# Performance work log

Measured on AMD Instinct MI355X. Metric: run time of the kernel, lower is better.

Reference implementation:

```python
import jax, jax.numpy as jnp
import numpy as np

INPUT_DIM = 1024
DAY_EMB = 8
PRED_LEN = 96
HIDDEN = 512
BATCH = 4096


def setup_inputs() -> dict:
    key = jax.random.key(0)
    ks = jax.random.split(key, 6)
    x = jax.random.normal(ks[0], (BATCH, INPUT_DIM), dtype=jnp.float32)
    day_emb = jax.random.normal(ks[1], (PRED_LEN, DAY_EMB), dtype=jnp.float32)
    # stacked per-head first-layer weights: in = input_dim + day_emb_dim
    W1 = jax.random.normal(ks[2], (PRED_LEN, INPUT_DIM + DAY_EMB, HIDDEN), dtype=jnp.float32) * 0.02
    b1 = jax.random.normal(ks[3], (PRED_LEN, HIDDEN), dtype=jnp.float32) * 0.02
    # stacked per-head output Linear(hidden, 1) weights (squeezed)
    W2 = jax.random.normal(ks[4], (PRED_LEN, HIDDEN), dtype=jnp.float32) * 0.02
    b2 = jax.random.normal(ks[5], (PRED_LEN,), dtype=jnp.float32) * 0.02
    return {"x": x, "day_emb": day_emb, "W1": W1, "b1": b1, "W2": W2, "b2": b2}


def reference(x, day_emb, W1, b1, W2, b2):
    # Each head p sees f = concat([x, day_emb[p]]) -> Linear -> ReLU -> (Dropout eval=id) -> Linear(.,1)
    # Split W1 into the x-part and emb-part so we never materialize the [P,B,in+emb] concat.
    W1x = W1[:, :INPUT_DIM, :]          # [P, D, H]
    W1e = W1[:, INPUT_DIM:, :]          # [P, E, H]
    h = jnp.einsum('bd,pdh->pbh', x, W1x)  # [P, B, H]
    h = h + (jnp.einsum('pe,peh->ph', day_emb, W1e) + b1)[:, None, :]
    h = jax.nn.relu(h)
    out = jnp.einsum('pbh,ph->pb', h, W2) + b2[:, None]  # [P, B]
    return out.T  # [B, pred_len]
```

## Files before the change

### kernel.cpp

```cpp
#include <hip/hip_runtime.h>
#include <hip/hip_bf16.h>
#include <stdint.h>

#define INPUT_DIM 1024
#define PRED_LEN 96
#define HIDDEN 512
#define BATCH 4096
#define W1_ROWS 1032

typedef __attribute__((ext_vector_type(8))) short bf16x8;
typedef __attribute__((ext_vector_type(4))) float floatx4;

__device__ __forceinline__ unsigned short f32_to_bf16_rne(float f) {
    union { float f; unsigned int u; } v; v.f = f;
    unsigned int u = v.u;
    unsigned int r = u + 0x7fffu + ((u >> 16) & 1u);
    return (unsigned short)(r >> 16);
}

__device__ __forceinline__ void async_copy16(const void* g, void* l) {
    __builtin_amdgcn_global_load_lds(
        (const __attribute__((address_space(1))) unsigned int*)g,
        (__attribute__((address_space(3))) unsigned int*)l, 16, 0, 0);
}

__global__ void convert_x_kernel(const float* __restrict__ x,
                                 unsigned short* __restrict__ xb) {
    int i = (blockIdx.x * 256 + threadIdx.x) * 4;
    float4 v = *reinterpret_cast<const float4*>(x + i);
    ushort4 o;
    o.x = f32_to_bf16_rne(v.x);
    o.y = f32_to_bf16_rne(v.y);
    o.z = f32_to_bf16_rne(v.z);
    o.w = f32_to_bf16_rne(v.w);
    *reinterpret_cast<ushort4*>(xb + i) = o;
}

__global__ void transpose_w1_kernel(const float* __restrict__ W1,
                                    unsigned short* __restrict__ W1t) {
    __shared__ unsigned short tile[64 * 64];
    int bid = blockIdx.x;
    int nt = bid & 7;
    int kt = (bid >> 3) & 15;
    int p  = bid >> 7;
    int t  = threadIdx.x;
    const float* src = W1 + (size_t)p * W1_ROWS * HIDDEN;
    const int k0 = kt * 64, n0 = nt * 64;

    const int tn = t & 15;
    const int tk = t >> 4;
    float4 v[4];
    #pragma unroll
    for (int i = 0; i < 4; ++i)
        v[i] = *reinterpret_cast<const float4*>(src + (size_t)(k0 + 4 * tk + i) * HIDDEN + n0 + 4 * tn);
    const int slot1 = ((tk >> 2) ^ (tn & 3)) * 16 + (tk & 3) * 4;
    {
        ushort4 w0, w1, w2, w3;
        w0.x = f32_to_bf16_rne(v[0].x); w0.y = f32_to_bf16_rne(v[1].x);
        w0.z = f32_to_bf16_rne(v[2].x); w0.w = f32_to_bf16_rne(v[3].x);
        w1.x = f32_to_bf16_rne(v[0].y); w1.y = f32_to_bf16_rne(v[1].y);
        w1.z = f32_to_bf16_rne(v[2].y); w1.w = f32_to_bf16_rne(v[3].y);
        w2.x = f32_to_bf16_rne(v[0].z); w2.y = f32_to_bf16_rne(v[1].z);
        w2.z = f32_to_bf16_rne(v[2].z); w2.w = f32_to_bf16_rne(v[3].z);
        w3.x = f32_to_bf16_rne(v[0].w); w3.y = f32_to_bf16_rne(v[1].w);
        w3.z = f32_to_bf16_rne(v[2].w); w3.w = f32_to_bf16_rne(v[3].w);
        *reinterpret_cast<ushort4*>(tile + (4 * tn + 0) * 64 + slot1) = w0;
        *reinterpret_cast<ushort4*>(tile + (4 * tn + 1) * 64 + slot1) = w1;
        *reinterpret_cast<ushort4*>(tile + (4 * tn + 2) * 64 + slot1) = w2;
        *reinterpret_cast<ushort4*>(tile + (4 * tn + 3) * 64 + slot1) = w3;
    }
    __syncthreads();

    const int nr = t >> 2;
    const int q  = t & 3;
    const int slot2 = (q ^ ((nr >> 2) & 3)) * 16;
    uint4 a = *reinterpret_cast<const uint4*>(tile + nr * 64 + slot2);
    uint4 b = *reinterpret_cast<const uint4*>(tile + nr * 64 + slot2 + 8);
    size_t dst = ((size_t)p * HIDDEN + n0 + nr) * 1024 + k0 + q * 16;
    *reinterpret_cast<uint4*>(W1t + dst)     = a;
    *reinterpret_cast<uint4*>(W1t + dst + 8) = b;
}

__global__ void bias_kernel(const float* __restrict__ W1,
                            const float* __restrict__ day_emb,
                            const float* __restrict__ b1,
                            float* __restrict__ bias) {
    int p = blockIdx.x;
    int h = threadIdx.x;
    const float* W1e = W1 + ((size_t)p * W1_ROWS + INPUT_DIM) * HIDDEN;
    float acc = b1[p * HIDDEN + h];
    #pragma unroll
    for (int e = 0; e < 8; ++e)
        acc += day_emb[p * 8 + e] * W1e[(size_t)e * HIDDEN + h];
    bias[p * HIDDEN + h] = acc;
}

__global__ void __launch_bounds__(256, 3)
mlp_head_kernel(const unsigned short* __restrict__ xb,
                const unsigned short* __restrict__ W1t,
                const float* __restrict__ bias,
                const float* __restrict__ W2,
                const float* __restrict__ b2,
                float* __restrict__ out)
{
    __shared__ unsigned short As[128 * 64];
    __shared__ unsigned short Bs[128 * 64];
    __shared__ float w2s[HIDDEN];
    __shared__ float biass[HIDDEN];
    __shared__ float red[2][128];

    const int mt   = blockIdx.x;
    const int p    = blockIdx.y;
    const int t    = threadIdx.x;
    const int lane = t & 63;
    const int w    = t >> 6;
    const int wi   = w >> 1;
    const int wj   = w & 1;
    const int l15  = lane & 15;
    const int quad = lane >> 4;
    const int xl   = l15 & 7;

    const int t3    = t >> 3;
    const int skc   = ((t & 7) ^ (t3 & 7)) * 8;
    const int ldsq8 = t * 8;

    for (int i = t; i < HIDDEN; i += 256) {
        w2s[i]   = W2[p * HIDDEN + i];
        biass[i] = bias[p * HIDDEN + i];
    }

    const int m0 = mt * 128;
    const unsigned short* ag = xb  + (size_t)m0 * 1024 + (size_t)t3 * 1024 + skc;
    const unsigned short* bg = W1t + (size_t)p * HIDDEN * 1024 + (size_t)t3 * 1024 + skc;

    float partial[4][4];
    #pragma unroll
    for (int i = 0; i < 4; ++i)
        #pragma unroll
        for (int r = 0; r < 4; ++r) partial[i][r] = 0.f;

    for (int nt = 0; nt < 4; ++nt) {
        floatx4 acc[4][4];
        #pragma unroll
        for (int i = 0; i < 4; ++i)
            #pragma unroll
            for (int j = 0; j < 4; ++j)
                acc[i][j] = (floatx4){0.f, 0.f, 0.f, 0.f};

        const size_t bn = (size_t)nt * 128 * 1024;

        for (int k0 = 0; k0 < 1024; k0 += 64) {
            __syncthreads();
            #pragma unroll
            for (int c = 0; c < 4; ++c) {
                async_copy16(ag + (size_t)c * 32 * 1024 + k0,      As + ldsq8 + c * 2048);
                async_copy16(bg + bn + (size_t)c * 32 * 1024 + k0, Bs + ldsq8 + c * 2048);
            }
            __syncthreads();
            #pragma unroll
            for (int kk = 0; kk < 2; ++kk) {
                const int slot = (kk * 4 + quad) ^ xl;
                bf16x8 af[4], bfr[4];
                #pragma unroll
                for (int i = 0; i < 4; ++i) {
                    int r = wi * 64 + i * 16 + l15;
                    af[i] = *reinterpret_cast<const bf16x8*>(As + r * 64 + slot * 8);
                }
                #pragma unroll
                for (int j = 0; j < 4; ++j) {
                    int n = wj * 64 + j * 16 + l15;
                    bfr[j] = *reinterpret_cast<const bf16x8*>(Bs + n * 64 + slot * 8);
                }
                #pragma unroll
                for (int i = 0; i < 4; ++i)
                    #pragma unroll
                    for (int j = 0; j < 4; ++j)
                        acc[i][j] = __builtin_amdgcn_mfma_f32_16x16x32_bf16(
                            af[i], bfr[j], acc[i][j], 0, 0, 0);
            }
        }

        const int n0 = nt * 128;
        #pragma unroll
        for (int j = 0; j < 4; ++j) {
            int c = n0 + wj * 64 + j * 16 + l15;
            float w2v = w2s[c];
            float bv  = biass[c];
            #pragma unroll
            for (int i = 0; i < 4; ++i)
                #pragma unroll
                for (int r = 0; r < 4; ++r) {
                    float hv = acc[i][j][r] + bv;
                    hv = hv > 0.f ? hv : 0.f;
                    partial[i][r] += hv * w2v;
                }
        }
    }

    #pragma unroll
    for (int i = 0; i < 4; ++i)
        #pragma unroll
        for (int r = 0; r < 4; ++r) {
            float v = partial[i][r];
            v += __shfl_xor(v, 1);
            v += __shfl_xor(v, 2);
            v += __shfl_xor(v, 4);
            v += __shfl_xor(v, 8);
            partial[i][r] = v;
        }

    if (l15 == 0) {
        #pragma unroll
        for (int i = 0; i < 4; ++i)
            #pragma unroll
            for (int r = 0; r < 4; ++r) {
                int row = wi * 64 + i * 16 + quad * 4 + r;
                red[wj][row] = partial[i][r];
            }
    }
    __syncthreads();
    if (t < 128) {
        float v = red[0][t] + red[1][t] + b2[p];
        out[(size_t)(m0 + t) * PRED_LEN + p] = v;
    }
}

extern "C" void kernel_launch(void* const* d_in, const int* in_sizes, int n_in,
                              void* d_out, int out_size, void* d_ws, size_t ws_size,
                              hipStream_t stream) {
    const float* x       = (const float*)d_in[0];
    const float* day_emb = (const float*)d_in[1];
    const float* W1      = (const float*)d_in[2];
    const float* b1      = (const float*)d_in[3];
    const float* W2      = (const float*)d_in[4];
    const float* b2      = (const float*)d_in[5];
    float* out = (float*)d_out;

    const size_t xb_bytes  = (size_t)BATCH * INPUT_DIM * 2;
    const size_t w1t_bytes = (size_t)PRED_LEN * HIDDEN * INPUT_DIM * 2;
    const size_t bias_bytes = (size_t)PRED_LEN * HIDDEN * 4;
    if (ws_size < xb_bytes + w1t_bytes + bias_bytes) return;

    unsigned short* xb  = (unsigned short*)d_ws;
    unsigned short* w1t = (unsigned short*)((char*)d_ws + xb_bytes);
    float* biasp        = (float*)((char*)d_ws + xb_bytes + w1t_bytes);

    convert_x_kernel<<<(BATCH * INPUT_DIM) / (256 * 4), 256, 0, stream>>>(x, xb);
    transpose_w1_kernel<<<PRED_LEN * 16 * 8, 256, 0, stream>>>(W1, w1t);
    bias_kernel<<<PRED_LEN, HIDDEN, 0, stream>>>(W1, day_emb, b1, biasp);

    dim3 grid(BATCH / 128, PRED_LEN);
    mlp_head_kernel<<<grid, 256, 0, stream>>>(xb, w1t, biasp, W2, b2, out);
}
```

Baseline: 678.0 us.

## Double-buffer LDS tiles with K-step 32 to overlap loads with MFMA

```diff
diff --git a/kernel.cpp b/kernel.cpp
--- a/kernel.cpp
+++ b/kernel.cpp
@@ -103,8 +103,8 @@
                 const float* __restrict__ b2,
                 float* __restrict__ out)
 {
-    __shared__ unsigned short As[128 * 64];
-    __shared__ unsigned short Bs[128 * 64];
+    __shared__ unsigned short As[2][128 * 32];
+    __shared__ unsigned short Bs[2][128 * 32];
     __shared__ float w2s[HIDDEN];
     __shared__ float biass[HIDDEN];
     __shared__ float red[2][128];
@@ -118,11 +118,11 @@
     const int wj   = w & 1;
     const int l15  = lane & 15;
     const int quad = lane >> 4;
-    const int xl   = l15 & 7;
-
-    const int t3    = t >> 3;
-    const int skc   = ((t & 7) ^ (t3 & 7)) * 8;
-    const int ldsq8 = t * 8;
+    const int slt  = quad ^ (l15 & 3);
+
+    const int r0   = t >> 2;
+    const int skc  = (((t & 3) ^ (r0 & 3))) * 8;
+    const int ldso = t * 8;
 
     for (int i = t; i < HIDDEN; i += 256) {
         w2s[i]   = W2[p * HIDDEN + i];
@@ -130,8 +130,8 @@
     }
 
     const int m0 = mt * 128;
-    const unsigned short* ag = xb  + (size_t)m0 * 1024 + (size_t)t3 * 1024 + skc;
-    const unsigned short* bg = W1t + (size_t)p * HIDDEN * 1024 + (size_t)t3 * 1024 + skc;
+    const unsigned short* ag = xb  + (size_t)(m0 + r0) * 1024 + skc;
+    const unsigned short* bg = W1t + ((size_t)p * HIDDEN + r0) * 1024 + skc;
 
     float partial[4][4];
     #pragma unroll
@@ -149,35 +149,40 @@
 
         const size_t bn = (size_t)nt * 128 * 1024;
 
-        for (int k0 = 0; k0 < 1024; k0 += 64) {
+        async_copy16(ag,                 As[0] + ldso);
+        async_copy16(ag + 64 * 1024,     As[0] + 2048 + ldso);
+        async_copy16(bg + bn,            Bs[0] + ldso);
+        async_copy16(bg + bn + 64 * 1024, Bs[0] + 2048 + ldso);
+        __syncthreads();
+
+        #pragma unroll 2
+        for (int ks = 0; ks < 32; ++ks) {
+            const int cur = ks & 1;
+            if (ks < 31) {
+                const int k0 = (ks + 1) * 32;
+                async_copy16(ag + k0,                  As[cur ^ 1] + ldso);
+                async_copy16(ag + 64 * 1024 + k0,      As[cur ^ 1] + 2048 + ldso);
+                async_copy16(bg + bn + k0,             Bs[cur ^ 1] + ldso);
+                async_copy16(bg + bn + 64 * 1024 + k0, Bs[cur ^ 1] + 2048 + ldso);
+            }
+            bf16x8 af[4], bfr[4];
+            #pragma unroll
+            for (int i = 0; i < 4; ++i) {
+                int r = wi * 64 + i * 16 + l15;
+                af[i] = *reinterpret_cast<const bf16x8*>(As[cur] + r * 32 + slt * 8);
+            }
+            #pragma unroll
+            for (int j = 0; j < 4; ++j) {
+                int n = wj * 64 + j * 16 + l15;
+                bfr[j] = *reinterpret_cast<const bf16x8*>(Bs[cur] + n * 32 + slt * 8);
+            }
+            #pragma unroll
+            for (int i = 0; i < 4; ++i)
+                #pragma unroll
+                for (int j = 0; j < 4; ++j)
+                    acc[i][j] = __builtin_amdgcn_mfma_f32_16x16x32_bf16(
+                        af[i], bfr[j], acc[i][j], 0, 0, 0);
             __syncthreads();
-            #pragma unroll
-            for (int c = 0; c < 4; ++c) {
-                async_copy16(ag + (size_t)c * 32 * 1024 + k0,      As + ldsq8 + c * 2048);
-                async_copy16(bg + bn + (size_t)c * 32 * 1024 + k0, Bs + ldsq8 + c * 2048);
-            }
-            __syncthreads();
-            #pragma unroll
-            for (int kk = 0; kk < 2; ++kk) {
-                const int slot = (kk * 4 + quad) ^ xl;
-                bf16x8 af[4], bfr[4];
-                #pragma unroll
-                for (int i = 0; i < 4; ++i) {
-                    int r = wi * 64 + i * 16 + l15;
-                    af[i] = *reinterpret_cast<const bf16x8*>(As + r * 64 + slot * 8);
-                }
-                #pragma unroll
-                for (int j = 0; j < 4; ++j) {
-                    int n = wj * 64 + j * 16 + l15;
-                    bfr[j] = *reinterpret_cast<const bf16x8*>(Bs + n * 64 + slot * 8);
-                }
-                #pragma unroll
-                for (int i = 0; i < 4; ++i)
-                    #pragma unroll
-                    for (int j = 0; j < 4; ++j)
-                        acc[i][j] = __builtin_amdgcn_mfma_f32_16x16x32_bf16(
-                            af[i], bfr[j], acc[i][j], 0, 0, 0);
-            }
         }
 
         const int n0 = nt * 128;
```

After: 975.6 us. 43.9% more time.

## Use 256x256 tiles with double-buffered LDS and interleaved MFMA/load phases

Applied to the files above, without the earlier changes.

```diff
diff --git a/kernel.cpp b/kernel.cpp
--- a/kernel.cpp
+++ b/kernel.cpp
@@ -95,7 +95,7 @@
     bias[p * HIDDEN + h] = acc;
 }
 
-__global__ void __launch_bounds__(256, 3)
+__global__ void __launch_bounds__(512, 2)
 mlp_head_kernel(const unsigned short* __restrict__ xb,
                 const unsigned short* __restrict__ W1t,
                 const float* __restrict__ bias,
@@ -103,91 +103,170 @@
                 const float* __restrict__ b2,
                 float* __restrict__ out)
 {
-    __shared__ unsigned short As[128 * 64];
-    __shared__ unsigned short Bs[128 * 64];
+    __shared__ unsigned short A_lds[2][256 * 64];
+    __shared__ unsigned short B_lds[2][256 * 64];
     __shared__ float w2s[HIDDEN];
     __shared__ float biass[HIDDEN];
-    __shared__ float red[2][128];
+    __shared__ float red[4][256];
 
     const int mt   = blockIdx.x;
     const int p    = blockIdx.y;
     const int t    = threadIdx.x;
     const int lane = t & 63;
     const int w    = t >> 6;
-    const int wi   = w >> 1;
-    const int wj   = w & 1;
+    const int wm   = w >> 2;
+    const int wn   = w & 3;
     const int l15  = lane & 15;
     const int quad = lane >> 4;
-    const int xl   = l15 & 7;
-
-    const int t3    = t >> 3;
-    const int skc   = ((t & 7) ^ (t3 & 7)) * 8;
-    const int ldsq8 = t * 8;
-
-    for (int i = t; i < HIDDEN; i += 256) {
+    const int sl0  = (quad ^ (l15 & 7)) * 8;
+    const int sl1  = ((4 + quad) ^ (l15 & 7)) * 8;
+
+    const int aro = (wm * 128 + l15) * 64;
+    const int bro = (wn * 64  + l15) * 64;
+
+    const int tr   = t >> 3;
+    const int skc  = ((t & 7) ^ (tr & 7)) * 8;
+    const int ldst = t * 8;
+
+    const int m0 = mt * 256;
+    const unsigned short* agb = xb  + (size_t)(m0 + tr) * 1024 + skc;
+    const unsigned short* bgb = W1t + ((size_t)p * HIDDEN + tr) * 1024 + skc;
+
+    for (int i = t; i < HIDDEN; i += 512) {
         w2s[i]   = W2[p * HIDDEN + i];
         biass[i] = bias[p * HIDDEN + i];
     }
-
-    const int m0 = mt * 128;
-    const unsigned short* ag = xb  + (size_t)m0 * 1024 + (size_t)t3 * 1024 + skc;
-    const unsigned short* bg = W1t + (size_t)p * HIDDEN * 1024 + (size_t)t3 * 1024 + skc;
-
-    float partial[4][4];
+    __syncthreads();
+
+    float partial[8][4];
     #pragma unroll
-    for (int i = 0; i < 4; ++i)
+    for (int i = 0; i < 8; ++i)
         #pragma unroll
         for (int r = 0; r < 4; ++r) partial[i][r] = 0.f;
 
-    for (int nt = 0; nt < 4; ++nt) {
-        floatx4 acc[4][4];
-        #pragma unroll
-        for (int i = 0; i < 4; ++i)
+    for (int nt = 0; nt < 2; ++nt) {
+        const size_t bnt = (size_t)nt * 256 * 1024;
+
+        floatx4 acc[8][4];
+        #pragma unroll
+        for (int i = 0; i < 8; ++i)
             #pragma unroll
             for (int j = 0; j < 4; ++j)
                 acc[i][j] = (floatx4){0.f, 0.f, 0.f, 0.f};
 
-        const size_t bn = (size_t)nt * 128 * 1024;
-
-        for (int k0 = 0; k0 < 1024; k0 += 64) {
-            __syncthreads();
-            #pragma unroll
-            for (int c = 0; c < 4; ++c) {
-                async_copy16(ag + (size_t)c * 32 * 1024 + k0,      As + ldsq8 + c * 2048);
-                async_copy16(bg + bn + (size_t)c * 32 * 1024 + k0, Bs + ldsq8 + c * 2048);
-            }
-            __syncthreads();
-            #pragma unroll
-            for (int kk = 0; kk < 2; ++kk) {
-                const int slot = (kk * 4 + quad) ^ xl;
-                bf16x8 af[4], bfr[4];
-                #pragma unroll
-                for (int i = 0; i < 4; ++i) {
-                    int r = wi * 64 + i * 16 + l15;
-                    af[i] = *reinterpret_cast<const bf16x8*>(As + r * 64 + slot * 8);
-                }
-                #pragma unroll
-                for (int j = 0; j < 4; ++j) {
-                    int n = wj * 64 + j * 16 + l15;
-                    bfr[j] = *reinterpret_cast<const bf16x8*>(Bs + n * 64 + slot * 8);
-                }
-                #pragma unroll
-                for (int i = 0; i < 4; ++i)
-                    #pragma unroll
-                    for (int j = 0; j < 4; ++j)
-                        acc[i][j] = __builtin_amdgcn_mfma_f32_16x16x32_bf16(
-                            af[i], bfr[j], acc[i][j], 0, 0, 0);
-            }
+        #pragma unroll
+        for (int part = 0; part < 4; ++part) {
+            async_copy16(agb + (size_t)part * 65536,       &A_lds[0][part * 4096 + ldst]);
+            async_copy16(bgb + bnt + (size_t)part * 65536, &B_lds[0][part * 4096 + ldst]);
         }
-
-        const int n0 = nt * 128;
+        asm volatile("s_waitcnt vmcnt(0)" ::: "memory");
+        __builtin_amdgcn_s_barrier();
+
+        for (int kt = 0; kt < 16; ++kt) {
+            const int cur = kt & 1;
+            const unsigned short* Ab = A_lds[cur];
+            const unsigned short* Bb = B_lds[cur];
+            unsigned short* An = A_lds[cur ^ 1];
+            unsigned short* Bn = B_lds[cur ^ 1];
+            const int kof = (kt + 1) * 64;
+            bf16x8 af[4][2], bf[2][2];
+
+            #pragma unroll
+            for (int i = 0; i < 4; ++i) {
+                af[i][0] = *reinterpret_cast<const bf16x8*>(Ab + aro + i * 1024 + sl0);
+                af[i][1] = *reinterpret_cast<const bf16x8*>(Ab + aro + i * 1024 + sl1);
+            }
+            #pragma unroll
+            for (int j = 0; j < 2; ++j) {
+                bf[j][0] = *reinterpret_cast<const bf16x8*>(Bb + bro + j * 1024 + sl0);
+                bf[j][1] = *reinterpret_cast<const bf16x8*>(Bb + bro + j * 1024 + sl1);
+            }
+            if (kt < 15) {
+                async_copy16(agb + kof,                &An[ldst]);
+                async_copy16(agb + 65536 + kof,        &An[4096 + ldst]);
+                async_copy16(bgb + bnt + kof,          &Bn[ldst]);
+                async_copy16(bgb + bnt + 65536 + kof,  &Bn[4096 + ldst]);
+            }
+            __builtin_amdgcn_s_barrier();
+            __builtin_amdgcn_s_setprio(1);
+            #pragma unroll
+            for (int i = 0; i < 4; ++i)
+                #pragma unroll
+                for (int j = 0; j < 2; ++j) {
+                    acc[i][j] = __builtin_amdgcn_mfma_f32_16x16x32_bf16(af[i][0], bf[j][0], acc[i][j], 0, 0, 0);
+                    acc[i][j] = __builtin_amdgcn_mfma_f32_16x16x32_bf16(af[i][1], bf[j][1], acc[i][j], 0, 0, 0);
+                }
+            __builtin_amdgcn_s_setprio(0);
+            __builtin_amdgcn_s_barrier();
+
+            #pragma unroll
+            for (int j = 0; j < 2; ++j) {
+                bf[j][0] = *reinterpret_cast<const bf16x8*>(Bb + bro + (j + 2) * 1024 + sl0);
+                bf[j][1] = *reinterpret_cast<const bf16x8*>(Bb + bro + (j + 2) * 1024 + sl1);
+            }
+            if (kt < 15) {
+                async_copy16(agb + 131072 + kof,       &An[8192 + ldst]);
+                async_copy16(agb + 196608 + kof,       &An[12288 + ldst]);
+                async_copy16(bgb + bnt + 131072 + kof, &Bn[8192 + ldst]);
+                async_copy16(bgb + bnt + 196608 + kof, &Bn[12288 + ldst]);
+            }
+            __builtin_amdgcn_s_barrier();
+            __builtin_amdgcn_s_setprio(1);
+            #pragma unroll
+            for (int i = 0; i < 4; ++i)
+                #pragma unroll
+                for (int j = 0; j < 2; ++j) {
+                    acc[i][j + 2] = __builtin_amdgcn_mfma_f32_16x16x32_bf16(af[i][0], bf[j][0], acc[i][j + 2], 0, 0, 0);
+                    acc[i][j + 2] = __builtin_amdgcn_mfma_f32_16x16x32_bf16(af[i][1], bf[j][1], acc[i][j + 2], 0, 0, 0);
+                }
+            __builtin_amdgcn_s_setprio(0);
+            __builtin_amdgcn_s_barrier();
+
+            #pragma unroll
+            for (int i = 0; i < 4; ++i) {
+                af[i][0] = *reinterpret_cast<const bf16x8*>(Ab + aro + (i + 4) * 1024 + sl0);
+                af[i][1] = *reinterpret_cast<const bf16x8*>(Ab + aro + (i + 4) * 1024 + sl1);
+            }
+            __builtin_amdgcn_s_barrier();
+            __builtin_amdgcn_s_setprio(1);
+            #pragma unroll
+            for (int i = 0; i < 4; ++i)
+                #pragma unroll
+                for (int j = 0; j < 2; ++j) {
+                    acc[i + 4][j + 2] = __builtin_amdgcn_mfma_f32_16x16x32_bf16(af[i][0], bf[j][0], acc[i + 4][j + 2], 0, 0, 0);
+                    acc[i + 4][j + 2] = __builtin_amdgcn_mfma_f32_16x16x32_bf16(af[i][1], bf[j][1], acc[i + 4][j + 2], 0, 0, 0);
+                }
+            __builtin_amdgcn_s_setprio(0);
+            __builtin_amdgcn_s_barrier();
+
+            #pragma unroll
+            for (int j = 0; j < 2; ++j) {
+                bf[j][0] = *reinterpret_cast<const bf16x8*>(Bb + bro + j * 1024 + sl0);
+                bf[j][1] = *reinterpret_cast<const bf16x8*>(Bb + bro + j * 1024 + sl1);
+            }
+            __builtin_amdgcn_s_barrier();
+            __builtin_amdgcn_s_setprio(1);
+            #pragma unroll
+            for (int i = 0; i < 4; ++i)
+                #pragma unroll
+                for (int j = 0; j < 2; ++j) {
+                    acc[i + 4][j] = __builtin_amdgcn_mfma_f32_16x16x32_bf16(af[i][0], bf[j][0], acc[i + 4][j], 0, 0, 0);
+                    acc[i + 4][j] = __builtin_amdgcn_mfma_f32_16x16x32_bf16(af[i][1], bf[j][1], acc[i + 4][j], 0, 0, 0);
+                }
+            __builtin_amdgcn_s_setprio(0);
+            if (kt < 15)
+                asm volatile("s_waitcnt vmcnt(0)" ::: "memory");
+            __builtin_amdgcn_s_barrier();
+        }
+
+        const int nb0 = nt * 256;
         #pragma unroll
         for (int j = 0; j < 4; ++j) {
-            int c = n0 + wj * 64 + j * 16 + l15;
+            int c = nb0 + wn * 64 + j * 16 + l15;
             float w2v = w2s[c];
             float bv  = biass[c];
             #pragma unroll
-            for (int i = 0; i < 4; ++i)
+            for (int i = 0; i < 8; ++i)
                 #pragma unroll
                 for (int r = 0; r < 4; ++r) {
                     float hv = acc[i][j][r] + bv;
@@ -198,7 +277,7 @@
     }
 
     #pragma unroll
-    for (int i = 0; i < 4; ++i)
+    for (int i = 0; i < 8; ++i)
         #pragma unroll
         for (int r = 0; r < 4; ++r) {
             float v = partial[i][r];
@@ -211,16 +290,16 @@
 
     if (l15 == 0) {
         #pragma unroll
-        for (int i = 0; i < 4; ++i)
+        for (int i = 0; i < 8; ++i)
             #pragma unroll
             for (int r = 0; r < 4; ++r) {
-                int row = wi * 64 + i * 16 + quad * 4 + r;
-                red[wj][row] = partial[i][r];
+                int row = wm * 128 + i * 16 + quad * 4 + r;
+                red[wn][row] = partial[i][r];
             }
     }
     __syncthreads();
-    if (t < 128) {
-        float v = red[0][t] + red[1][t] + b2[p];
+    if (t < 256) {
+        float v = red[0][t] + red[1][t] + red[2][t] + red[3][t] + b2[p];
         out[(size_t)(m0 + t) * PRED_LEN + p] = v;
     }
 }
@@ -249,6 +328,6 @@
     transpose_w1_kernel<<<PRED_LEN * 16 * 8, 256, 0, stream>>>(W1, w1t);
     bias_kernel<<<PRED_LEN, HIDDEN, 0, stream>>>(W1, day_emb, b1, biasp);
 
-    dim3 grid(BATCH / 128, PRED_LEN);
-    mlp_head_kernel<<<grid, 256, 0, stream>>>(xb, w1t, biasp, W2, b2, out);
-}
+    dim3 grid(BATCH / 256, PRED_LEN);
+    mlp_head_kernel<<<grid, 512, 0, stream>>>(xb, w1t, biasp, W2, b2, out);
+}
```

Result: no change. 676.4 us (-0.2%).
